# Kernel optimization log

Hardware: AMD Instinct MI355X
Metric: run time of the kernel (lower is better)

## Reference

```python
import jax, jax.numpy as jnp
import numpy as np

B, S, H, HD, DM = 8, 1024, 16, 64, 1024

def rotate_half(x):
    x1, x2 = x[..., : x.shape[-1] // 2], x[..., x.shape[-1] // 2 :]
    return jnp.concatenate((-x2, x1), axis=-1)

def apply_rope(x, cos, sin):
    return x * cos + rotate_half(x) * sin

def setup_inputs() -> dict:
    key = jax.random.key(0)
    ks = jax.random.split(key, 6)
    T = B * S
    hidden_states = jax.random.normal(ks[0], (T, DM), dtype=jnp.float32)
    scale = 1.0 / np.sqrt(DM)
    q_w = jax.random.normal(ks[1], (DM, DM), dtype=jnp.float32) * scale
    k_w = jax.random.normal(ks[2], (DM, DM), dtype=jnp.float32) * scale
    v_w = jax.random.normal(ks[3], (DM, DM), dtype=jnp.float32) * scale
    o_w = jax.random.normal(ks[4], (DM, DM), dtype=jnp.float32) * scale
    # RoPE tables: positions restart at each segment boundary
    pos = jnp.tile(jnp.arange(S, dtype=jnp.float32), B)           # [T]
    inv_freq = 1.0 / (10000.0 ** (jnp.arange(0, HD, 2, dtype=jnp.float32) / HD))
    ang = pos[:, None] * inv_freq[None, :]                        # [T, HD/2]
    emb = jnp.concatenate([ang, ang], axis=-1)                    # [T, HD]
    cos = jnp.cos(emb)[:, None, :]                                # [T, 1, HD]
    sin = jnp.sin(emb)[:, None, :]
    cu_seqlens = (jnp.arange(B + 1) * S).astype(jnp.int32)        # [B+1]
    return {
        "hidden_states": hidden_states,
        "q_w": q_w, "k_w": k_w, "v_w": v_w, "o_w": o_w,
        "cos": cos, "sin": sin,
        "cu_seqlens": cu_seqlens, "max_seqlen": S,
    }

def reference(hidden_states, q_w, k_w, v_w, o_w, cos, sin, cu_seqlens, max_seqlen):
    T, D = hidden_states.shape
    hd = cos.shape[-1]
    nh = D // hd
    nb = cu_seqlens.shape[0] - 1
    S_ = max_seqlen
    # QKV projections (torch Linear: y = x @ W^T)
    q = (hidden_states @ q_w.T).reshape(T, nh, hd)
    k = (hidden_states @ k_w.T).reshape(T, nh, hd)
    v = (hidden_states @ v_w.T).reshape(T, nh, hd)
    q = apply_rope(q, cos, sin)
    k = apply_rope(k, cos, sin)
    # Equal-length varlen segments -> dense batched causal attention
    q = q.reshape(nb, S_, nh, hd)
    k = k.reshape(nb, S_, nh, hd)
    v = v.reshape(nb, S_, nh, hd)
    scale = 1.0 / np.sqrt(hd).astype(np.float32)
    scores = jnp.einsum("bqhd,bkhd->bhqk", q, k) * scale          # [B,H,S,S]
    causal = jnp.tril(jnp.ones((S_, S_), dtype=bool))
    scores = jnp.where(causal[None, None], scores, jnp.finfo(scores.dtype).min)
    probs = jax.nn.softmax(scores, axis=-1)
    attn = jnp.einsum("bhqk,bkhd->bqhd", probs, v).reshape(T, D)
    return attn @ o_w.T
```

## Files before the change

### kernel.cpp

```cpp
#include <hip/hip_runtime.h>

typedef __attribute__((ext_vector_type(8))) short short8;
typedef __attribute__((ext_vector_type(4))) short short4v;
typedef __attribute__((ext_vector_type(4))) float f32x4;

#define MFMA(a, b, c) __builtin_amdgcn_mfma_f32_16x16x32_bf16((a), (b), (c), 0, 0, 0)
#define GLD16(g, l)                                                            \
  __builtin_amdgcn_global_load_lds(                                            \
      (const __attribute__((address_space(1))) void*)(g),                      \
      (__attribute__((address_space(3))) void*)(l), 16, 0, 0)

static __device__ __forceinline__ float b2f(unsigned short b) {
  union { unsigned u; float f; } u; u.u = ((unsigned)b) << 16; return u.f;
}
static __device__ __forceinline__ unsigned short f2b(float f) {
  union { float f; unsigned u; } u; u.f = f;
  unsigned r = u.u + 0x7FFFu + ((u.u >> 16) & 1u);
  return (unsigned short)(r >> 16);
}

__global__ __launch_bounds__(256) void convert_kernel(
    const float* __restrict__ hidden,
    const float* __restrict__ qw, const float* __restrict__ kw,
    const float* __restrict__ vw, const float* __restrict__ ow,
    unsigned short* __restrict__ dst) {
  const int HID4 = 2097152, W4 = 262144, TOT = HID4 + 4 * W4;
  for (int i = blockIdx.x * 256 + threadIdx.x; i < TOT; i += gridDim.x * 256) {
    const float* src; int off;
    if (i < HID4) { src = hidden; off = i; }
    else {
      int j = i - HID4; int w = j >> 18; off = j & (W4 - 1);
      src = (w == 0) ? qw : (w == 1) ? kw : (w == 2) ? vw : ow;
    }
    float4 v = *(const float4*)&src[(size_t)off * 4];
    short4v s;
    s[0] = (short)f2b(v.x); s[1] = (short)f2b(v.y);
    s[2] = (short)f2b(v.z); s[3] = (short)f2b(v.w);
    *(short4v*)&dst[(size_t)i * 4] = s;
  }
}

template <bool QKV>
__global__ __launch_bounds__(512, 2) void gemm256(
    const unsigned short* __restrict__ A,
    const unsigned short* __restrict__ W,
    void* __restrict__ Cv,
    const float* __restrict__ cosb, const float* __restrict__ sinb) {
  __shared__ __align__(16) unsigned short lds[73728];
  const int tid = threadIdx.x, wave = tid >> 6, lane = tid & 63;
  const int bm = blockIdx.x << 8, bnc = blockIdx.y << 7;
  const int wr = (wave >> 1) << 6, wc = (wave & 1) << 6;
  const int lr = lane & 15, hi4 = lane >> 4;
  const int rowb = tid >> 3;
  const int cgA = (tid & 7) ^ (rowb & 7);
  const unsigned short* aSrc = A + (size_t)(bm + rowb) * 1024 + (cgA << 3);
  const unsigned short* bSrc = W + (size_t)(bnc + rowb) * 1024 + (cgA << 3);

  f32x4 acc[4][4] = {};

#define STAGE(t, bi)                                                           \
  do {                                                                         \
    unsigned short* As_ = lds + (bi) * 24576;                                  \
    unsigned short* Bs_ = As_ + 16384;                                         \
    const int k0_ = (t) << 6;                                                  \
    _Pragma("unroll") for (int i = 0; i < 4; ++i)                              \
        GLD16(aSrc + (size_t)(i << 6) * 1024 + k0_,                            \
              As_ + (((i << 9) + tid) << 3));                                  \
    _Pragma("unroll") for (int j = 0; j < 2; ++j)                              \
        GLD16(bSrc + (size_t)(j << 6) * 1024 + k0_,                            \
              Bs_ + (((j << 9) + tid) << 3));                                  \
  } while (0)

  STAGE(0, 0);
  STAGE(1, 1);
  asm volatile("s_waitcnt vmcnt(6)" ::: "memory");
  __builtin_amdgcn_s_barrier();
  __builtin_amdgcn_sched_barrier(0);

  int bi = 0;
#pragma unroll
  for (int t = 0; t < 16; ++t) {
    int pf = bi + 2; if (pf >= 3) pf -= 3;
    if (t < 14) STAGE(t + 2, pf);
    const unsigned short* As = lds + bi * 24576;
    const unsigned short* Bs = As + 16384;
    short8 af[2][4], bfr[2][4];
#pragma unroll
    for (int kk = 0; kk < 2; ++kk)
#pragma unroll
      for (int x = 0; x < 4; ++x) {
        int ra = wr + x * 16 + lr;
        af[kk][x] = *(const short8*)&As[ra * 64 + (((hi4 + kk * 4) ^ (ra & 7)) << 3)];
        int rb = wc + x * 16 + lr;
        bfr[kk][x] = *(const short8*)&Bs[rb * 64 + (((hi4 + kk * 4) ^ (rb & 7)) << 3)];
      }
    __builtin_amdgcn_s_setprio(1);
#pragma unroll
    for (int kk = 0; kk < 2; ++kk)
#pragma unroll
      for (int mm = 0; mm < 4; ++mm)
#pragma unroll
        for (int nn = 0; nn < 4; ++nn)
          acc[mm][nn] = MFMA(af[kk][mm], bfr[kk][nn], acc[mm][nn]);
    __builtin_amdgcn_s_setprio(0);
    __builtin_amdgcn_sched_barrier(0);
    if (t < 14) asm volatile("s_waitcnt vmcnt(6)" ::: "memory");
    else        asm volatile("s_waitcnt vmcnt(0)" ::: "memory");
    __builtin_amdgcn_s_barrier();
    __builtin_amdgcn_sched_barrier(0);
    if (++bi == 3) bi = 0;
  }
#undef STAGE

  const int rg = hi4 << 2;
  if constexpr (QKV) {
    const int grp = bnc >> 10;
    unsigned short* Cbuf = (unsigned short*)Cv + (size_t)grp * 8388608;
    const int colbase = (bnc & 1023) + wc;
    if (grp < 2) {
      float* csf = (float*)lds;
      float* snf = csf + 8192;
#pragma unroll
      for (int i = 0; i < 4; ++i) {
        int s = (i << 9) + tid;
        int row = s >> 3, c4 = (s & 7) << 2;
        GLD16(cosb + (size_t)(bm + row) * 64 + c4, csf + s * 4);
        GLD16(sinb + (size_t)(bm + row) * 64 + c4, snf + s * 4);
      }
      asm volatile("s_waitcnt vmcnt(0)" ::: "memory");
      __builtin_amdgcn_s_barrier();
      __builtin_amdgcn_sched_barrier(0);
      const float sc = (grp == 0) ? 0.18033688011112042f : 1.0f;
#pragma unroll
      for (int mm = 0; mm < 4; ++mm)
#pragma unroll
        for (int r = 0; r < 4; ++r) {
          int rloc = wr + mm * 16 + rg + r;
          size_t rowoff = (size_t)(bm + rloc) * 1024;
#pragma unroll
          for (int nn = 0; nn < 2; ++nn) {
            int d = nn * 16 + lr;
            float c = csf[rloc * 32 + d], s2 = snf[rloc * 32 + d];
            float lo = acc[mm][nn][r], hi = acc[mm][nn + 2][r];
            Cbuf[rowoff + colbase + nn * 16 + lr]      = f2b((lo * c - hi * s2) * sc);
            Cbuf[rowoff + colbase + nn * 16 + lr + 32] = f2b((hi * c + lo * s2) * sc);
          }
        }
    } else {
#pragma unroll
      for (int mm = 0; mm < 4; ++mm)
#pragma unroll
        for (int nn = 0; nn < 4; ++nn)
#pragma unroll
          for (int r = 0; r < 4; ++r)
            Cbuf[(size_t)(bm + wr + mm * 16 + rg + r) * 1024 + colbase + nn * 16 + lr] =
                f2b(acc[mm][nn][r]);
    }
  } else {
    float* C = (float*)Cv;
#pragma unroll
    for (int mm = 0; mm < 4; ++mm)
#pragma unroll
      for (int nn = 0; nn < 4; ++nn)
#pragma unroll
        for (int r = 0; r < 4; ++r)
          C[(size_t)(bm + wr + mm * 16 + rg + r) * 1024 + bnc + wc + nn * 16 + lr] =
              acc[mm][nn][r];
  }
}

__global__ __launch_bounds__(256, 3) void attn_kernel(
    const unsigned short* __restrict__ Q,
    const unsigned short* __restrict__ K,
    const unsigned short* __restrict__ V,
    unsigned short* __restrict__ O) {
  __shared__ unsigned short Ks[2][64][72];
  __shared__ unsigned short Vt[2][64][72];
  const int tid = threadIdx.x, wave = tid >> 6, lane = tid & 63;
  const int idx = blockIdx.x;
  const int bh = idx & 127;
  const int b = bh >> 4, h = bh & 15;
  const int qb = 7 - (idx >> 7);
  const int tok0 = b << 10;
  const int lr = lane & 15, hi4 = lane >> 4, lk8 = hi4 << 3;
  const int rg = hi4 << 2;
  const int qrow0 = (qb << 7) + (wave << 5);

  short8 qf[2][2];
#pragma unroll
  for (int mt = 0; mt < 2; ++mt) {
    const unsigned short* qp = &Q[(size_t)(tok0 + qrow0 + mt * 16 + lr) * 1024 + h * 64];
#pragma unroll
    for (int kk = 0; kk < 2; ++kk) qf[mt][kk] = *(const short8*)&qp[kk * 32 + lk8];
  }

  f32x4 acc[2][4] = {};
  float m[2], l[2];
#pragma unroll
  for (int mt = 0; mt < 2; ++mt) { m[mt] = -1e30f; l[mt] = 0.f; }

  const int krow = tid >> 3, kcol = (tid & 7) << 3;
  const int vd = lane;
  const int baseC = ((wave & 1) << 4) + ((wave >> 1) << 2);
  short8 kst[2];
  short4v vst[4];

#define LOADT(kbx)                                                                 \
  do {                                                                             \
    const int kr0_ = tok0 + ((kbx) << 6);                                          \
    _Pragma("unroll") for (int it = 0; it < 2; ++it)                               \
        kst[it] = *(const short8*)&K[(size_t)(kr0_ + krow + it * 32) * 1024 +      \
                                     h * 64 + kcol];                               \
    _Pragma("unroll") for (int it = 0; it < 2; ++it) {                             \
      const unsigned short* vp_ =                                                  \
          &V[(size_t)(kr0_ + ((wave + it * 4) << 3)) * 1024 + h * 64 + vd];        \
      _Pragma("unroll") for (int i = 0; i < 4; ++i) {                              \
        vst[it * 2][i]     = (short)vp_[(size_t)i * 1024];                         \
        vst[it * 2 + 1][i] = (short)vp_[(size_t)(i + 4) * 1024];                   \
      }                                                                            \
    }                                                                              \
  } while (0)

#define STORET(bi)                                                                 \
  do {                                                                             \
    _Pragma("unroll") for (int it = 0; it < 2; ++it)                               \
        *(short8*)&Ks[bi][krow + it * 32][kcol] = kst[it];                         \
    *(short4v*)&Vt[bi][vd][baseC]          = vst[0];                               \
    *(short4v*)&Vt[bi][vd][baseC + 8]      = vst[1];                               \
    *(short4v*)&Vt[bi][vd][32 + baseC]     = vst[2];                               \
    *(short4v*)&Vt[bi][vd][32 + baseC + 8] = vst[3];                               \
  } while (0)

  const int nkb = (qb + 1) << 1;
  LOADT(0);
  STORET(0);
  __syncthreads();

  for (int kb = 0; kb < nkb; ++kb) {
    const int cur = kb & 1;
    const bool more = (kb + 1 < nkb);
    if (more) LOADT(kb + 1);

#pragma unroll
    for (int mt = 0; mt < 2; ++mt) {
      float p[4][4];
#pragma unroll
      for (int ct = 0; ct < 4; ++ct) {
        short8 kf0 = *(const short8*)&Ks[cur][ct * 16 + lr][lk8];
        short8 kf1 = *(const short8*)&Ks[cur][ct * 16 + lr][32 + lk8];
        f32x4 s = {};
        s = MFMA(kf0, qf[mt][0], s);
        s = MFMA(kf1, qf[mt][1], s);
#pragma unroll
        for (int r = 0; r < 4; ++r) p[ct][r] = s[r];
      }
      if (kb >= 2 * qb) {
        const int qg = qrow0 + mt * 16 + lr;
#pragma unroll
        for (int ct = 0; ct < 4; ++ct)
#pragma unroll
          for (int r = 0; r < 4; ++r) {
            int kg = (kb << 6) + ct * 16 + rg + r;
            if (kg > qg) p[ct][r] = -1e30f;
          }
      }
      float mx = p[0][0];
#pragma unroll
      for (int ct = 0; ct < 4; ++ct)
#pragma unroll
        for (int r = 0; r < 4; ++r) mx = fmaxf(mx, p[ct][r]);
      mx = fmaxf(mx, __shfl_xor(mx, 16));
      mx = fmaxf(mx, __shfl_xor(mx, 32));
      if (__any(mx > m[mt] + 8.f)) {
        float mn = fmaxf(m[mt], mx);
        float alpha = __builtin_amdgcn_exp2f(m[mt] - mn);
        m[mt] = mn;
        l[mt] *= alpha;
        float a4[4];
#pragma unroll
        for (int r = 0; r < 4; ++r) a4[r] = __shfl(alpha, rg + r);
#pragma unroll
        for (int dt = 0; dt < 4; ++dt)
#pragma unroll
          for (int r = 0; r < 4; ++r) acc[mt][dt][r] *= a4[r];
      }
      unsigned pk[4][2];
      float rs = 0.f;
#pragma unroll
      for (int ct = 0; ct < 4; ++ct) {
#pragma unroll
        for (int r = 0; r < 4; ++r) {
          p[ct][r] = __builtin_amdgcn_exp2f(p[ct][r] - m[mt]);
          rs += p[ct][r];
        }
        pk[ct][0] = ((unsigned)f2b(p[ct][1]) << 16) | f2b(p[ct][0]);
        pk[ct][1] = ((unsigned)f2b(p[ct][3]) << 16) | f2b(p[ct][2]);
      }
#pragma unroll
      for (int kk = 0; kk < 2; ++kk) {
        union { unsigned u[4]; short8 v; } pa;
        pa.u[0] = pk[kk * 2][0];
        pa.u[1] = pk[kk * 2][1];
        pa.u[2] = pk[kk * 2 + 1][0];
        pa.u[3] = pk[kk * 2 + 1][1];
#pragma unroll
        for (int dt = 0; dt < 4; ++dt) {
          short8 vf = *(const short8*)&Vt[cur][dt * 16 + lr][kk * 32 + lk8];
          acc[mt][dt] = MFMA(pa.v, vf, acc[mt][dt]);
        }
      }
      rs += __shfl_xor(rs, 16);
      rs += __shfl_xor(rs, 32);
      l[mt] += rs;
    }

    if (more) {
      STORET(cur ^ 1);
      __syncthreads();
    }
  }
#undef LOADT
#undef STORET

#pragma unroll
  for (int mt = 0; mt < 2; ++mt) {
    float linv = 1.0f / l[mt];
    float inv[4];
#pragma unroll
    for (int r = 0; r < 4; ++r) inv[r] = __shfl(linv, rg + r);
#pragma unroll
    for (int dt = 0; dt < 4; ++dt)
#pragma unroll
      for (int r = 0; r < 4; ++r) {
        int trow = tok0 + qrow0 + mt * 16 + rg + r;
        O[(size_t)trow * 1024 + h * 64 + dt * 16 + lr] = f2b(acc[mt][dt][r] * inv[r]);
      }
  }
}

extern "C" void kernel_launch(void* const* d_in, const int* in_sizes, int n_in,
                              void* d_out, int out_size, void* d_ws, size_t ws_size,
                              hipStream_t stream) {
  const float* hidden = (const float*)d_in[0];
  const float* q_w    = (const float*)d_in[1];
  const float* k_w    = (const float*)d_in[2];
  const float* v_w    = (const float*)d_in[3];
  const float* o_w    = (const float*)d_in[4];
  const float* cosb   = (const float*)d_in[5];
  const float* sinb   = (const float*)d_in[6];

  const size_t TD = (size_t)8192 * 1024;
  unsigned short* ws  = (unsigned short*)d_ws;
  unsigned short* Qb  = ws;
  unsigned short* Kb  = ws + TD;
  unsigned short* Vb  = ws + 2 * TD;
  unsigned short* hBF = ws + 3 * TD;
  unsigned short* wBF = ws + 4 * TD;

  convert_kernel<<<4096, 256, 0, stream>>>(hidden, q_w, k_w, v_w, o_w, hBF);
  gemm256<true><<<dim3(32, 24), 512, 0, stream>>>(hBF, wBF, Qb, cosb, sinb);
  attn_kernel<<<1024, 256, 0, stream>>>(Qb, Kb, Vb, hBF );
  gemm256<false><<<dim3(32, 8), 512, 0, stream>>>(
      hBF, wBF + 3 * 1048576, d_out, nullptr, nullptr);
}
```

Before: 139.8 us.

## Split GEMM K-tile into two half-phases interleaving LDS reads, prefetch, and MFMA

Restructures the main GEMM loop so each 64-wide K tile is handled in two half-phases. Each phase loads half the A/B fragments from LDS, issues part of the next tile's global-to-LDS prefetch, synchronises with a barrier, then runs 16 MFMAs. This spreads the global loads and LDS reads across the MFMA work and lowers live fragment registers, aiming to improve overlap. In exchange it adds an extra barrier per tile.

```diff
diff --git a/kernel.cpp b/kernel.cpp
--- a/kernel.cpp
+++ b/kernel.cpp
@@ -81,27 +81,64 @@
 #pragma unroll
   for (int t = 0; t < 16; ++t) {
     int pf = bi + 2; if (pf >= 3) pf -= 3;
-    if (t < 14) STAGE(t + 2, pf);
     const unsigned short* As = lds + bi * 24576;
     const unsigned short* Bs = As + 16384;
-    short8 af[2][4], bfr[2][4];
-#pragma unroll
-    for (int kk = 0; kk < 2; ++kk)
-#pragma unroll
-      for (int x = 0; x < 4; ++x) {
-        int ra = wr + x * 16 + lr;
-        af[kk][x] = *(const short8*)&As[ra * 64 + (((hi4 + kk * 4) ^ (ra & 7)) << 3)];
-        int rb = wc + x * 16 + lr;
-        bfr[kk][x] = *(const short8*)&Bs[rb * 64 + (((hi4 + kk * 4) ^ (rb & 7)) << 3)];
-      }
+    unsigned short* Asp = lds + pf * 24576;
+    unsigned short* Bsp = Asp + 16384;
+    const int k2 = (t + 2) << 6;
+
+    short8 afA[4], bfA[4];
+#pragma unroll
+    for (int x = 0; x < 4; ++x) {
+      int ra = wr + x * 16 + lr;
+      afA[x] = *(const short8*)&As[ra * 64 + ((hi4 ^ (ra & 7)) << 3)];
+      int rb = wc + x * 16 + lr;
+      bfA[x] = *(const short8*)&Bs[rb * 64 + ((hi4 ^ (rb & 7)) << 3)];
+    }
+    if (t < 14) {
+#pragma unroll
+      for (int i = 0; i < 2; ++i)
+        GLD16(aSrc + (size_t)(i << 6) * 1024 + k2, Asp + (((i << 9) + tid) << 3));
+      GLD16(bSrc + k2, Bsp + (tid << 3));
+    }
+    __builtin_amdgcn_sched_barrier(0);
+    __builtin_amdgcn_s_barrier();
+    asm volatile("s_waitcnt lgkmcnt(0)" ::: "memory");
+    __builtin_amdgcn_sched_barrier(0);
     __builtin_amdgcn_s_setprio(1);
 #pragma unroll
-    for (int kk = 0; kk < 2; ++kk)
-#pragma unroll
-      for (int mm = 0; mm < 4; ++mm)
-#pragma unroll
-        for (int nn = 0; nn < 4; ++nn)
-          acc[mm][nn] = MFMA(af[kk][mm], bfr[kk][nn], acc[mm][nn]);
+    for (int mm = 0; mm < 4; ++mm)
+#pragma unroll
+      for (int nn = 0; nn < 4; ++nn)
+        acc[mm][nn] = MFMA(afA[mm], bfA[nn], acc[mm][nn]);
+    __builtin_amdgcn_s_setprio(0);
+    __builtin_amdgcn_sched_barrier(0);
+    __builtin_amdgcn_s_barrier();
+
+    short8 afB[4], bfB[4];
+#pragma unroll
+    for (int x = 0; x < 4; ++x) {
+      int ra = wr + x * 16 + lr;
+      afB[x] = *(const short8*)&As[ra * 64 + (((hi4 + 4) ^ (ra & 7)) << 3)];
+      int rb = wc + x * 16 + lr;
+      bfB[x] = *(const short8*)&Bs[rb * 64 + (((hi4 + 4) ^ (rb & 7)) << 3)];
+    }
+    if (t < 14) {
+#pragma unroll
+      for (int i = 2; i < 4; ++i)
+        GLD16(aSrc + (size_t)(i << 6) * 1024 + k2, Asp + (((i << 9) + tid) << 3));
+      GLD16(bSrc + (size_t)(1 << 6) * 1024 + k2, Bsp + (((1 << 9) + tid) << 3));
+    }
+    __builtin_amdgcn_sched_barrier(0);
+    __builtin_amdgcn_s_barrier();
+    asm volatile("s_waitcnt lgkmcnt(0)" ::: "memory");
+    __builtin_amdgcn_sched_barrier(0);
+    __builtin_amdgcn_s_setprio(1);
+#pragma unroll
+    for (int mm = 0; mm < 4; ++mm)
+#pragma unroll
+      for (int nn = 0; nn < 4; ++nn)
+        acc[mm][nn] = MFMA(afB[mm], bfB[nn], acc[mm][nn]);
     __builtin_amdgcn_s_setprio(0);
     __builtin_amdgcn_sched_barrier(0);
     if (t < 14) asm volatile("s_waitcnt vmcnt(6)" ::: "memory");
```

Result: faster. 137.1 us (-2.0%).
